# Kernel tuning notes

Measured on AMD Instinct MI355X. Metric: run time of the kernel, lower is better.

The kernel has to match this reference:

```python
import jax, jax.numpy as jnp
import numpy as np

NUM_HEADS = 16
ROPE_BASE = 10000.0


def _rope_interleaved(x, cos, sin):
    # x: [B,S,H,Hd]; cos/sin: [S,Hd/2]. Interleaved pairs (even, odd).
    x1 = x[..., 0::2]
    x2 = x[..., 1::2]
    c = cos[None, :, None, :]
    s = sin[None, :, None, :]
    o1 = x1 * c - x2 * s
    o2 = x1 * s + x2 * c
    return jnp.stack([o1, o2], axis=-1).reshape(x.shape)


def setup_inputs() -> dict:
    key = jax.random.key(0)
    ks = jax.random.split(key, 5)
    B, S, D = 2, 2048, 2048
    init_scale = 0.02
    x = jax.random.normal(ks[0], (B, S, D), jnp.float32)
    Wq = jax.random.normal(ks[1], (D, D), jnp.float32) * init_scale
    Wk = jax.random.normal(ks[2], (D, D), jnp.float32) * init_scale
    Wv = jax.random.normal(ks[3], (D, D), jnp.float32) * init_scale
    Wo = jax.random.normal(ks[4], (D, D), jnp.float32) * init_scale
    return {"x": x, "Wq": Wq, "Wk": Wk, "Wv": Wv, "Wo": Wo}


def reference(x, Wq, Wk, Wv, Wo):
    B, S, D = x.shape
    H = NUM_HEADS
    Hd = D // H
    # QKV projections (bias-free)
    q = (x @ Wq).reshape(B, S, H, Hd)
    k = (x @ Wk).reshape(B, S, H, Hd)
    v = (x @ Wv).reshape(B, S, H, Hd)
    # Rotary embedding, interleaved, base 10000, full head_dim
    pos = jnp.arange(S, dtype=jnp.float32)
    inv_freq = 1.0 / (ROPE_BASE ** (jnp.arange(0, Hd, 2, dtype=jnp.float32) / Hd))
    angles = pos[:, None] * inv_freq[None, :]  # [S, Hd/2]
    cos, sin = jnp.cos(angles), jnp.sin(angles)
    q = _rope_interleaved(q, cos, sin)
    k = _rope_interleaved(k, cos, sin)
    # Causal scaled-dot-product attention (flash_attn_func default scale = Hd**-0.5)
    scale = Hd ** -0.5
    scores = jnp.einsum('bqhd,bkhd->bhqk', q, k) * scale
    causal = jnp.tril(jnp.ones((S, S), dtype=bool))
    scores = jnp.where(causal[None, None], scores, jnp.finfo(scores.dtype).min)
    probs = jax.nn.softmax(scores, axis=-1)
    attn = jnp.einsum('bhqk,bkhd->bqhd', probs, v).reshape(B, S, D)
    return attn @ Wo
```

## Files before the change

kernel.cpp:

```cpp
#include <hip/hip_runtime.h>
#include <hip/hip_bf16.h>

static constexpr int BB = 2;
static constexpr int SS = 2048;
static constexpr int DD = 2048;
static constexpr int HH = 16;
static constexpr int HD = 128;

typedef __bf16 bf16_t;
typedef __bf16 bf16x8 __attribute__((ext_vector_type(8)));
typedef __bf16 bf16x4 __attribute__((ext_vector_type(4)));
typedef float  floatx4 __attribute__((ext_vector_type(4)));

__device__ __forceinline__ void gl2lds16(const bf16_t* g, bf16_t* l) {
    __builtin_amdgcn_global_load_lds(
        (const __attribute__((address_space(1))) void*)g,
        (__attribute__((address_space(3))) void*)l, 16, 0, 0);
}

__global__ void cast_x_kernel(const float* __restrict__ x, bf16_t* __restrict__ xb) {
    int i = blockIdx.x * 256 + threadIdx.x;
    float4 v = ((const float4*)x)[i];
    bf16x4 o;
    o.x = (bf16_t)v.x; o.y = (bf16_t)v.y; o.z = (bf16_t)v.z; o.w = (bf16_t)v.w;
    ((bf16x4*)xb)[i] = o;
}

__global__ void transpose_cast_kernel(const float* __restrict__ W, bf16_t* __restrict__ Wt) {
    __shared__ float tile[32][33];
    int bx = blockIdx.x * 32;
    int by = blockIdx.y * 32;
    int tx = threadIdx.x, ty = threadIdx.y;
#pragma unroll
    for (int j = 0; j < 4; ++j)
        tile[ty + j * 8][tx] = W[(size_t)(by + ty + j * 8) * DD + bx + tx];
    __syncthreads();
#pragma unroll
    for (int j = 0; j < 4; ++j)
        Wt[(size_t)(bx + ty + j * 8) * DD + by + tx] = (bf16_t)tile[tx][ty + j * 8];
}

template <int MODE>
__global__ __launch_bounds__(256, 2) void gemm_bt_kernel(
    const bf16_t* __restrict__ A, const bf16_t* __restrict__ Bt,
    float* __restrict__ Cf, bf16_t* __restrict__ Qw, bf16_t* __restrict__ Kw,
    bf16_t* __restrict__ Vtw, int N, int K) {
    __shared__ __align__(16) bf16_t As[128 * 64];
    __shared__ __align__(16) bf16_t Bs[128 * 64];

    const int t = threadIdx.x;
    const int lane = t & 63;
    const int wave = t >> 6;
    const int lrow = lane & 15;
    const int lkq  = lane >> 4;
    const int wm = (wave & 1) * 64;
    const int wn = (wave >> 1) * 64;
    const int m0 = blockIdx.y * 128;
    const int n0 = blockIdx.x * 128;

    floatx4 acc[4][4];
#pragma unroll
    for (int i = 0; i < 4; ++i)
#pragma unroll
        for (int j = 0; j < 4; ++j) acc[i][j] = (floatx4)0.0f;

    const int srow  = lane >> 3;
    const int sch   = (lane & 7) ^ srow;

    for (int k0 = 0; k0 < K; k0 += 64) {
        __syncthreads();
#pragma unroll
        for (int p = 0; p < 4; ++p) {
            int r = wave * 32 + p * 8 + srow;
            gl2lds16(A  + (size_t)(m0 + r) * K + k0 + sch * 8, As + (wave * 32 + p * 8) * 64);
            gl2lds16(Bt + (size_t)(n0 + r) * K + k0 + sch * 8, Bs + (wave * 32 + p * 8) * 64);
        }
        __syncthreads();
#pragma unroll
        for (int ks = 0; ks < 2; ++ks) {
            bf16x8 af[4], bg[4];
#pragma unroll
            for (int i = 0; i < 4; ++i) {
                int pos = ((ks * 4 + lkq) ^ (lrow & 7)) * 8;
                af[i] = *(const bf16x8*)(As + (wm + i * 16 + lrow) * 64 + pos);
                bg[i] = *(const bf16x8*)(Bs + (wn + i * 16 + lrow) * 64 + pos);
            }
#pragma unroll
            for (int i = 0; i < 4; ++i)
#pragma unroll
                for (int j = 0; j < 4; ++j)
                    acc[i][j] = __builtin_amdgcn_mfma_f32_16x16x32_bf16(af[i], bg[j], acc[i][j], 0, 0, 0);
        }
    }

#pragma unroll
    for (int i = 0; i < 4; ++i)
#pragma unroll
        for (int j = 0; j < 4; ++j)
#pragma unroll
            for (int r = 0; r < 4; ++r) {
                int m = m0 + wm + i * 16 + lkq * 4 + r;
                int n = n0 + wn + j * 16 + lrow;
                float v = acc[i][j][r];
                if (MODE == 1) {
                    Cf[(size_t)m * N + n] = v;
                } else {
                    bf16_t bv = (bf16_t)v;
                    int b = m >> 11, s = m & (SS - 1);
                    if (n < DD) {
                        int h = n >> 7, d = n & 127;
                        Qw[(((size_t)b * HH + h) * SS + s) * HD + d] = bv;
                    } else if (n < 2 * DD) {
                        int nn = n - DD;
                        int h = nn >> 7, d = nn & 127;
                        Kw[(((size_t)b * HH + h) * SS + s) * HD + d] = bv;
                    } else {
                        int nn = n - 2 * DD;
                        int h = nn >> 7, d = nn & 127;
                        Vtw[(((size_t)b * HH + h) * HD + d) * SS + s] = bv;
                    }
                }
            }
}

__global__ void rope_kernel(bf16_t* __restrict__ Qw, bf16_t* __restrict__ Kw) {
    int idx = blockIdx.x * 256 + threadIdx.x;
    int i  = idx & 63;
    int s  = (idx >> 6) & (SS - 1);
    int bh = idx >> 17;
    float inv = expf(-(float)(2 * i) * (9.210340371976184f / 128.0f));
    float ang = (float)s * inv;
    float c = cosf(ang), sn = sinf(ang);
    size_t base = ((size_t)bh * SS + s) * HD + 2 * i;
    float q1 = (float)Qw[base], q2 = (float)Qw[base + 1];
    Qw[base]     = (bf16_t)(q1 * c - q2 * sn);
    Qw[base + 1] = (bf16_t)(q1 * sn + q2 * c);
    float k1 = (float)Kw[base], k2 = (float)Kw[base + 1];
    Kw[base]     = (bf16_t)(k1 * c - k2 * sn);
    Kw[base + 1] = (bf16_t)(k1 * sn + k2 * c);
}

__global__ __launch_bounds__(256, 3) void flash_attn_kernel(
    const bf16_t* __restrict__ Qw, const bf16_t* __restrict__ Kw,
    const bf16_t* __restrict__ Vtw, bf16_t* __restrict__ Attn) {
    __shared__ __align__(16) bf16_t Ks[64 * 128];
    __shared__ __align__(16) bf16_t Vs[128 * 64];
    __shared__ __align__(16) bf16_t Ps[4][16 * 72];

    const int t = threadIdx.x;
    const int lane = t & 63;
    const int wave = t >> 6;
    const int lrow = lane & 15;
    const int lkq  = lane >> 4;
    const int bx = blockIdx.x;
    const int qtile = (bx & 1) ? (bx >> 1) : (15 - (bx >> 1));
    const int bh = blockIdx.y;
    const int q0 = qtile * 128;

    const bf16_t* Qbh = Qw + (size_t)bh * SS * HD;
    const bf16_t* Kbh = Kw + (size_t)bh * SS * HD;
    const bf16_t* Vbh = Vtw + (size_t)bh * HD * SS;

    const int qb[2] = { q0 + wave * 16, q0 + 64 + wave * 16 };

    const float qscale = 0.08838834764831845f * 1.4426950408889634f;
    bf16x8 qf[2][4];
#pragma unroll
    for (int qs = 0; qs < 2; ++qs)
#pragma unroll
        for (int kc4 = 0; kc4 < 4; ++kc4) {
            qf[qs][kc4] = *(const bf16x8*)(Qbh + (size_t)(qb[qs] + lrow) * HD + kc4 * 32 + lkq * 8);
#pragma unroll
            for (int e = 0; e < 8; ++e) qf[qs][kc4][e] = (bf16_t)((float)qf[qs][kc4][e] * qscale);
        }

    floatx4 oacc[2][8];
#pragma unroll
    for (int qs = 0; qs < 2; ++qs)
#pragma unroll
        for (int i = 0; i < 8; ++i) oacc[qs][i] = (floatx4)0.0f;
    float m_i[2] = { -1e30f, -1e30f };
    float l_i[2] = { 0.0f, 0.0f };

    const int nch = 2 * qtile + 2;
    for (int kc = 0; kc < nch; ++kc) {
        __syncthreads();
#pragma unroll
        for (int p = 0; p < 4; ++p) {
            int row = wave * 16 + p * 4 + (lane >> 4);
            int gch = (lane & 15) ^ (row & 7);
            gl2lds16(Kbh + (size_t)(kc * 64 + row) * HD + gch * 8,
                     Ks + (wave * 16 + p * 4) * 128);
        }
#pragma unroll
        for (int p = 0; p < 4; ++p) {
            int row = wave * 32 + p * 8 + (lane >> 3);
            int gch = (lane & 7) ^ (row & 7);
            gl2lds16(Vbh + (size_t)row * SS + kc * 64 + gch * 8,
                     Vs + (wave * 32 + p * 8) * 64);
        }
        __syncthreads();

#pragma unroll
        for (int qs = 0; qs < 2; ++qs) {
            const int qbase = qb[qs];
            if (kc * 64 > qbase + 15) continue;

            floatx4 sacc[4];
#pragma unroll
            for (int i = 0; i < 4; ++i) sacc[i] = (floatx4)0.0f;
#pragma unroll
            for (int nf = 0; nf < 4; ++nf)
#pragma unroll
                for (int kc4 = 0; kc4 < 4; ++kc4) {
                    bf16x8 kf = *(const bf16x8*)(Ks + (nf * 16 + lrow) * 128 +
                                                 (((kc4 * 4 + lkq) ^ (lrow & 7)) * 8));
                    sacc[nf] = __builtin_amdgcn_mfma_f32_16x16x32_bf16(kf, qf[qs][kc4], sacc[nf], 0, 0, 0);
                }

            const int qg = qbase + lrow;
            float mx = m_i[qs];
            if (kc * 64 + 63 > qbase) {
#pragma unroll
                for (int nf = 0; nf < 4; ++nf)
#pragma unroll
                    for (int r = 0; r < 4; ++r) {
                        int kg = kc * 64 + nf * 16 + lkq * 4 + r;
                        float sv = (kg > qg) ? -1e30f : sacc[nf][r];
                        sacc[nf][r] = sv;
                        mx = fmaxf(mx, sv);
                    }
            } else {
#pragma unroll
                for (int nf = 0; nf < 4; ++nf)
#pragma unroll
                    for (int r = 0; r < 4; ++r) mx = fmaxf(mx, sacc[nf][r]);
            }
            mx = fmaxf(mx, __shfl_xor(mx, 16));
            mx = fmaxf(mx, __shfl_xor(mx, 32));
            float alpha = exp2f(m_i[qs] - mx);
            m_i[qs] = mx;

            float rs = 0.0f;
#pragma unroll
            for (int nf = 0; nf < 4; ++nf)
#pragma unroll
                for (int r = 0; r < 4; ++r) {
                    float pv = exp2f(sacc[nf][r] - mx);
                    sacc[nf][r] = pv;
                    rs += pv;
                }
            rs += __shfl_xor(rs, 16);
            rs += __shfl_xor(rs, 32);
            l_i[qs] = l_i[qs] * alpha + rs;

            float av[4];
#pragma unroll
            for (int r = 0; r < 4; ++r) av[r] = __shfl(alpha, lkq * 4 + r);
#pragma unroll
            for (int nf8 = 0; nf8 < 8; ++nf8)
#pragma unroll
                for (int r = 0; r < 4; ++r) oacc[qs][nf8][r] *= av[r];

#pragma unroll
            for (int nf = 0; nf < 4; ++nf) {
                bf16x4 pk;
#pragma unroll
                for (int r = 0; r < 4; ++r) pk[r] = (bf16_t)sacc[nf][r];
                *(bf16x4*)(Ps[wave] + lrow * 72 + nf * 16 + lkq * 4) = pk;
            }

            bf16x8 pa[2];
#pragma unroll
            for (int k2 = 0; k2 < 2; ++k2)
                pa[k2] = *(const bf16x8*)(Ps[wave] + lrow * 72 + k2 * 32 + lkq * 8);
#pragma unroll
            for (int nf8 = 0; nf8 < 8; ++nf8)
#pragma unroll
                for (int k2 = 0; k2 < 2; ++k2) {
                    bf16x8 vb = *(const bf16x8*)(Vs + (nf8 * 16 + lrow) * 64 +
                                                 (((k2 * 4 + lkq) ^ (lrow & 7)) * 8));
                    oacc[qs][nf8] = __builtin_amdgcn_mfma_f32_16x16x32_bf16(pa[k2], vb, oacc[qs][nf8], 0, 0, 0);
                }
        }
    }

    int bb = bh >> 4, h = bh & 15;
#pragma unroll
    for (int qs = 0; qs < 2; ++qs)
#pragma unroll
        for (int r = 0; r < 4; ++r) {
            float invl = 1.0f / __shfl(l_i[qs], lkq * 4 + r);
            int q = qb[qs] + lkq * 4 + r;
#pragma unroll
            for (int nf8 = 0; nf8 < 8; ++nf8)
                Attn[((size_t)bb * SS + q) * DD + h * HD + nf8 * 16 + lrow] =
                    (bf16_t)(oacc[qs][nf8][r] * invl);
        }
}

extern "C" void kernel_launch(void* const* d_in, const int* in_sizes, int n_in,
                              void* d_out, int out_size, void* d_ws, size_t ws_size,
                              hipStream_t stream) {
    const float* x  = (const float*)d_in[0];
    const float* Wq = (const float*)d_in[1];
    const float* Wk = (const float*)d_in[2];
    const float* Wv = (const float*)d_in[3];
    const float* Wo = (const float*)d_in[4];
    float* out = (float*)d_out;

    bf16_t* p = (bf16_t*)d_ws;
    bf16_t* Xb    = p; p += (size_t)BB * SS * DD;
    bf16_t* Wqkvt = p; p += (size_t)3 * DD * DD;
    bf16_t* Wot   = p; p += (size_t)DD * DD;
    bf16_t* Qw    = p; p += (size_t)BB * HH * SS * HD;
    bf16_t* Kw    = p; p += (size_t)BB * HH * SS * HD;
    bf16_t* Vtw   = p; p += (size_t)BB * HH * SS * HD;
    bf16_t* Attn  = p; p += (size_t)BB * SS * DD;

    cast_x_kernel<<<(BB * SS * DD / 4) / 256, 256, 0, stream>>>(x, Xb);

    dim3 tb(32, 8), tg(DD / 32, DD / 32);
    transpose_cast_kernel<<<tg, tb, 0, stream>>>(Wq, Wqkvt);
    transpose_cast_kernel<<<tg, tb, 0, stream>>>(Wk, Wqkvt + (size_t)DD * DD);
    transpose_cast_kernel<<<tg, tb, 0, stream>>>(Wv, Wqkvt + (size_t)2 * DD * DD);
    transpose_cast_kernel<<<tg, tb, 0, stream>>>(Wo, Wot);

    gemm_bt_kernel<0><<<dim3(3 * DD / 128, BB * SS / 128), 256, 0, stream>>>(
        Xb, Wqkvt, nullptr, Qw, Kw, Vtw, 3 * DD, DD);

    rope_kernel<<<(BB * HH * SS * 64) / 256, 256, 0, stream>>>(Qw, Kw);

    flash_attn_kernel<<<dim3(SS / 128, BB * HH), 256, 0, stream>>>(Qw, Kw, Vtw, Attn);

    gemm_bt_kernel<1><<<dim3(DD / 128, BB * SS / 128), 256, 0, stream>>>(
        Attn, Wot, out, nullptr, nullptr, nullptr, DD, DD);
}
```

Before: 445.5 us.

## Load K/V fragments directly into registers, dropping shared-memory staging in flash attention

The flash attention loop no longer stages K and V tiles through LDS with block-wide barriers. Each wave now loads its K and V MFMA fragments straight from global memory into registers and reuses them for both query sub-tiles. The rescale of the output accumulator is skipped when no lane's running max changed. This removes two __syncthreads per chunk and the LDS round trip, but every wave now fetches the full K/V tile from global memory or L2 (four times the global traffic), and register pressure grows, so launch bounds drop from 3 to 2 blocks.

```diff
diff --git a/kernel.cpp b/kernel.cpp
--- a/kernel.cpp
+++ b/kernel.cpp
@@ -140,11 +140,9 @@
     Kw[base + 1] = (bf16_t)(k1 * sn + k2 * c);
 }
 
-__global__ __launch_bounds__(256, 3) void flash_attn_kernel(
+__global__ __launch_bounds__(256, 2) void flash_attn_kernel(
     const bf16_t* __restrict__ Qw, const bf16_t* __restrict__ Kw,
     const bf16_t* __restrict__ Vtw, bf16_t* __restrict__ Attn) {
-    __shared__ __align__(16) bf16_t Ks[64 * 128];
-    __shared__ __align__(16) bf16_t Vs[128 * 64];
     __shared__ __align__(16) bf16_t Ps[4][16 * 72];
 
     const int t = threadIdx.x;
@@ -184,39 +182,42 @@
 
     const int nch = 2 * qtile + 2;
     for (int kc = 0; kc < nch; ++kc) {
-        __syncthreads();
-#pragma unroll
-        for (int p = 0; p < 4; ++p) {
-            int row = wave * 16 + p * 4 + (lane >> 4);
-            int gch = (lane & 15) ^ (row & 7);
-            gl2lds16(Kbh + (size_t)(kc * 64 + row) * HD + gch * 8,
-                     Ks + (wave * 16 + p * 4) * 128);
-        }
-#pragma unroll
-        for (int p = 0; p < 4; ++p) {
-            int row = wave * 32 + p * 8 + (lane >> 3);
-            int gch = (lane & 7) ^ (row & 7);
-            gl2lds16(Vbh + (size_t)row * SS + kc * 64 + gch * 8,
-                     Vs + (wave * 32 + p * 8) * 64);
-        }
-        __syncthreads();
+        bf16x8 kf[4][4];
+#pragma unroll
+        for (int nf = 0; nf < 4; ++nf)
+#pragma unroll
+            for (int kc4 = 0; kc4 < 4; ++kc4)
+                kf[nf][kc4] = *(const bf16x8*)(Kbh + (size_t)(kc * 64 + nf * 16 + lrow) * HD +
+                                               kc4 * 32 + lkq * 8);
+
+        const bool act0 = (kc * 64 <= qb[0] + 15);
+
+        floatx4 sacc[2][4];
+#pragma unroll
+        for (int qs = 0; qs < 2; ++qs)
+#pragma unroll
+            for (int i = 0; i < 4; ++i) sacc[qs][i] = (floatx4)0.0f;
+#pragma unroll
+        for (int nf = 0; nf < 4; ++nf)
+#pragma unroll
+            for (int kc4 = 0; kc4 < 4; ++kc4) {
+                if (act0)
+                    sacc[0][nf] = __builtin_amdgcn_mfma_f32_16x16x32_bf16(kf[nf][kc4], qf[0][kc4], sacc[0][nf], 0, 0, 0);
+                sacc[1][nf] = __builtin_amdgcn_mfma_f32_16x16x32_bf16(kf[nf][kc4], qf[1][kc4], sacc[1][nf], 0, 0, 0);
+            }
+
+        bf16x8 vf[8][2];
+#pragma unroll
+        for (int nf8 = 0; nf8 < 8; ++nf8)
+#pragma unroll
+            for (int k2 = 0; k2 < 2; ++k2)
+                vf[nf8][k2] = *(const bf16x8*)(Vbh + (size_t)(nf8 * 16 + lrow) * SS +
+                                               kc * 64 + k2 * 32 + lkq * 8);
 
 #pragma unroll
         for (int qs = 0; qs < 2; ++qs) {
             const int qbase = qb[qs];
-            if (kc * 64 > qbase + 15) continue;
-
-            floatx4 sacc[4];
-#pragma unroll
-            for (int i = 0; i < 4; ++i) sacc[i] = (floatx4)0.0f;
-#pragma unroll
-            for (int nf = 0; nf < 4; ++nf)
-#pragma unroll
-                for (int kc4 = 0; kc4 < 4; ++kc4) {
-                    bf16x8 kf = *(const bf16x8*)(Ks + (nf * 16 + lrow) * 128 +
-                                                 (((kc4 * 4 + lkq) ^ (lrow & 7)) * 8));
-                    sacc[nf] = __builtin_amdgcn_mfma_f32_16x16x32_bf16(kf, qf[qs][kc4], sacc[nf], 0, 0, 0);
-                }
+            if (qs == 0 && !act0) continue;
 
             const int qg = qbase + lrow;
             float mx = m_i[qs];
@@ -226,15 +227,15 @@
 #pragma unroll
                     for (int r = 0; r < 4; ++r) {
                         int kg = kc * 64 + nf * 16 + lkq * 4 + r;
-                        float sv = (kg > qg) ? -1e30f : sacc[nf][r];
-                        sacc[nf][r] = sv;
+                        float sv = (kg > qg) ? -1e30f : sacc[qs][nf][r];
+                        sacc[qs][nf][r] = sv;
                         mx = fmaxf(mx, sv);
                     }
             } else {
 #pragma unroll
                 for (int nf = 0; nf < 4; ++nf)
 #pragma unroll
-                    for (int r = 0; r < 4; ++r) mx = fmaxf(mx, sacc[nf][r]);
+                    for (int r = 0; r < 4; ++r) mx = fmaxf(mx, sacc[qs][nf][r]);
             }
             mx = fmaxf(mx, __shfl_xor(mx, 16));
             mx = fmaxf(mx, __shfl_xor(mx, 32));
@@ -246,27 +247,29 @@
             for (int nf = 0; nf < 4; ++nf)
 #pragma unroll
                 for (int r = 0; r < 4; ++r) {
-                    float pv = exp2f(sacc[nf][r] - mx);
-                    sacc[nf][r] = pv;
+                    float pv = exp2f(sacc[qs][nf][r] - mx);
+                    sacc[qs][nf][r] = pv;
                     rs += pv;
                 }
             rs += __shfl_xor(rs, 16);
             rs += __shfl_xor(rs, 32);
             l_i[qs] = l_i[qs] * alpha + rs;
 
-            float av[4];
-#pragma unroll
-            for (int r = 0; r < 4; ++r) av[r] = __shfl(alpha, lkq * 4 + r);
-#pragma unroll
-            for (int nf8 = 0; nf8 < 8; ++nf8)
-#pragma unroll
-                for (int r = 0; r < 4; ++r) oacc[qs][nf8][r] *= av[r];
+            if (__ballot(alpha < 1.0f)) {
+                float av[4];
+#pragma unroll
+                for (int r = 0; r < 4; ++r) av[r] = __shfl(alpha, lkq * 4 + r);
+#pragma unroll
+                for (int nf8 = 0; nf8 < 8; ++nf8)
+#pragma unroll
+                    for (int r = 0; r < 4; ++r) oacc[qs][nf8][r] *= av[r];
+            }
 
 #pragma unroll
             for (int nf = 0; nf < 4; ++nf) {
                 bf16x4 pk;
 #pragma unroll
-                for (int r = 0; r < 4; ++r) pk[r] = (bf16_t)sacc[nf][r];
+                for (int r = 0; r < 4; ++r) pk[r] = (bf16_t)sacc[qs][nf][r];
                 *(bf16x4*)(Ps[wave] + lrow * 72 + nf * 16 + lkq * 4) = pk;
             }
 
@@ -277,11 +280,8 @@
 #pragma unroll
             for (int nf8 = 0; nf8 < 8; ++nf8)
 #pragma unroll
-                for (int k2 = 0; k2 < 2; ++k2) {
-                    bf16x8 vb = *(const bf16x8*)(Vs + (nf8 * 16 + lrow) * 64 +
-                                                 (((k2 * 4 + lkq) ^ (lrow & 7)) * 8));
-                    oacc[qs][nf8] = __builtin_amdgcn_mfma_f32_16x16x32_bf16(pa[k2], vb, oacc[qs][nf8], 0, 0, 0);
-                }
+                for (int k2 = 0; k2 < 2; ++k2)
+                    oacc[qs][nf8] = __builtin_amdgcn_mfma_f32_16x16x32_bf16(pa[k2], vf[nf8][k2], oacc[qs][nf8], 0, 0, 0);
         }
     }
 
```

Result: slower. 562.2 us (+26.2%).

## Interleave two q-subtiles in flash attention, skip no-op rescale, separate V transpose

Applied to the files above, without the earlier changes.

The QKV GEMM now writes V in row-major head layout, so its epilogue no longer does strided scattered stores, and a separate tiled LDS kernel transposes V into the layout attention expects. The attention inner loop now computes both q-subtiles' QK and PV MFMAs together, sharing each K/V fragment load across two accumulators. It also skips the output rescale when no lane's running max changed. This adds a kernel launch and an extra pass over V, and lowers launch bounds occupancy from 3 to 2 blocks per CU to make room for more live registers.

```diff
diff --git a/kernel.cpp b/kernel.cpp
--- a/kernel.cpp
+++ b/kernel.cpp
@@ -44,7 +44,7 @@
 __global__ __launch_bounds__(256, 2) void gemm_bt_kernel(
     const bf16_t* __restrict__ A, const bf16_t* __restrict__ Bt,
     float* __restrict__ Cf, bf16_t* __restrict__ Qw, bf16_t* __restrict__ Kw,
-    bf16_t* __restrict__ Vtw, int N, int K) {
+    bf16_t* __restrict__ Vw, int N, int K) {
     __shared__ __align__(16) bf16_t As[128 * 64];
     __shared__ __align__(16) bf16_t Bs[128 * 64];
 
@@ -107,18 +107,12 @@
                 } else {
                     bf16_t bv = (bf16_t)v;
                     int b = m >> 11, s = m & (SS - 1);
-                    if (n < DD) {
-                        int h = n >> 7, d = n & 127;
-                        Qw[(((size_t)b * HH + h) * SS + s) * HD + d] = bv;
-                    } else if (n < 2 * DD) {
-                        int nn = n - DD;
-                        int h = nn >> 7, d = nn & 127;
-                        Kw[(((size_t)b * HH + h) * SS + s) * HD + d] = bv;
-                    } else {
-                        int nn = n - 2 * DD;
-                        int h = nn >> 7, d = nn & 127;
-                        Vtw[(((size_t)b * HH + h) * HD + d) * SS + s] = bv;
-                    }
+                    int nn = n & (DD - 1);
+                    int h = nn >> 7, d = nn & 127;
+                    size_t off = (((size_t)b * HH + h) * SS + s) * HD + d;
+                    if (n < DD)            Qw[off] = bv;
+                    else if (n < 2 * DD)   Kw[off] = bv;
+                    else                   Vw[off] = bv;
                 }
             }
 }
@@ -140,7 +134,34 @@
     Kw[base + 1] = (bf16_t)(k1 * sn + k2 * c);
 }
 
-__global__ __launch_bounds__(256, 3) void flash_attn_kernel(
+__global__ void vtrans_kernel(const bf16_t* __restrict__ Vw, bf16_t* __restrict__ Vt) {
+    __shared__ unsigned short lds[64][65];
+    const int t = threadIdx.x;
+    const int s0 = blockIdx.x * 64, d0 = blockIdx.y * 64, bh = blockIdx.z;
+    const bf16_t* src = Vw + ((size_t)bh * SS + s0) * HD + d0;
+    bf16_t* dst = Vt + ((size_t)bh * HD + d0) * SS + s0;
+#pragma unroll
+    for (int p = 0; p < 2; ++p) {
+        int c = p * 256 + t;
+        int s = c >> 3, ch = c & 7;
+        uint4 v = *(const uint4*)(src + (size_t)s * HD + ch * 8);
+        const unsigned short* pv = (const unsigned short*)&v;
+#pragma unroll
+        for (int e = 0; e < 8; ++e) lds[ch * 8 + e][s] = pv[e];
+    }
+    __syncthreads();
+    {
+        int d = t >> 2, sb = (t & 3) * 16;
+        uint4 o[2];
+        unsigned short* po = (unsigned short*)o;
+#pragma unroll
+        for (int e = 0; e < 16; ++e) po[e] = lds[d][sb + e];
+        *(uint4*)(dst + (size_t)d * SS + sb) = o[0];
+        *(uint4*)(dst + (size_t)d * SS + sb + 8) = o[1];
+    }
+}
+
+__global__ __launch_bounds__(256, 2) void flash_attn_kernel(
     const bf16_t* __restrict__ Qw, const bf16_t* __restrict__ Kw,
     const bf16_t* __restrict__ Vtw, bf16_t* __restrict__ Attn) {
     __shared__ __align__(16) bf16_t Ks[64 * 128];
@@ -201,22 +222,29 @@
         }
         __syncthreads();
 
+        const bool act0 = (kc * 64 <= qb[0] + 15);
+
+        floatx4 sacc[2][4];
+#pragma unroll
+        for (int qs = 0; qs < 2; ++qs)
+#pragma unroll
+            for (int i = 0; i < 4; ++i) sacc[qs][i] = (floatx4)0.0f;
+#pragma unroll
+        for (int nf = 0; nf < 4; ++nf)
+#pragma unroll
+            for (int kc4 = 0; kc4 < 4; ++kc4) {
+                bf16x8 kf = *(const bf16x8*)(Ks + (nf * 16 + lrow) * 128 +
+                                             (((kc4 * 4 + lkq) ^ (lrow & 7)) * 8));
+                if (act0)
+                    sacc[0][nf] = __builtin_amdgcn_mfma_f32_16x16x32_bf16(kf, qf[0][kc4], sacc[0][nf], 0, 0, 0);
+                sacc[1][nf] = __builtin_amdgcn_mfma_f32_16x16x32_bf16(kf, qf[1][kc4], sacc[1][nf], 0, 0, 0);
+            }
+
+        bf16x8 pa[2][2];
 #pragma unroll
         for (int qs = 0; qs < 2; ++qs) {
             const int qbase = qb[qs];
-            if (kc * 64 > qbase + 15) continue;
-
-            floatx4 sacc[4];
-#pragma unroll
-            for (int i = 0; i < 4; ++i) sacc[i] = (floatx4)0.0f;
-#pragma unroll
-            for (int nf = 0; nf < 4; ++nf)
-#pragma unroll
-                for (int kc4 = 0; kc4 < 4; ++kc4) {
-                    bf16x8 kf = *(const bf16x8*)(Ks + (nf * 16 + lrow) * 128 +
-                                                 (((kc4 * 4 + lkq) ^ (lrow & 7)) * 8));
-                    sacc[nf] = __builtin_amdgcn_mfma_f32_16x16x32_bf16(kf, qf[qs][kc4], sacc[nf], 0, 0, 0);
-                }
+            if (qs == 0 && !act0) continue;
 
             const int qg = qbase + lrow;
             float mx = m_i[qs];
@@ -226,15 +254,15 @@
 #pragma unroll
                     for (int r = 0; r < 4; ++r) {
                         int kg = kc * 64 + nf * 16 + lkq * 4 + r;
-                        float sv = (kg > qg) ? -1e30f : sacc[nf][r];
-                        sacc[nf][r] = sv;
+                        float sv = (kg > qg) ? -1e30f : sacc[qs][nf][r];
+                        sacc[qs][nf][r] = sv;
                         mx = fmaxf(mx, sv);
                     }
             } else {
 #pragma unroll
                 for (int nf = 0; nf < 4; ++nf)
 #pragma unroll
-                    for (int r = 0; r < 4; ++r) mx = fmaxf(mx, sacc[nf][r]);
+                    for (int r = 0; r < 4; ++r) mx = fmaxf(mx, sacc[qs][nf][r]);
             }
             mx = fmaxf(mx, __shfl_xor(mx, 16));
             mx = fmaxf(mx, __shfl_xor(mx, 32));
@@ -246,43 +274,46 @@
             for (int nf = 0; nf < 4; ++nf)
 #pragma unroll
                 for (int r = 0; r < 4; ++r) {
-                    float pv = exp2f(sacc[nf][r] - mx);
-                    sacc[nf][r] = pv;
+                    float pv = exp2f(sacc[qs][nf][r] - mx);
+                    sacc[qs][nf][r] = pv;
                     rs += pv;
                 }
             rs += __shfl_xor(rs, 16);
             rs += __shfl_xor(rs, 32);
             l_i[qs] = l_i[qs] * alpha + rs;
 
-            float av[4];
-#pragma unroll
-            for (int r = 0; r < 4; ++r) av[r] = __shfl(alpha, lkq * 4 + r);
-#pragma unroll
-            for (int nf8 = 0; nf8 < 8; ++nf8)
-#pragma unroll
-                for (int r = 0; r < 4; ++r) oacc[qs][nf8][r] *= av[r];
+            if (__ballot(alpha < 1.0f)) {
+                float av[4];
+#pragma unroll
+                for (int r = 0; r < 4; ++r) av[r] = __shfl(alpha, lkq * 4 + r);
+#pragma unroll
+                for (int nf8 = 0; nf8 < 8; ++nf8)
+#pragma unroll
+                    for (int r = 0; r < 4; ++r) oacc[qs][nf8][r] *= av[r];
+            }
 
 #pragma unroll
             for (int nf = 0; nf < 4; ++nf) {
                 bf16x4 pk;
 #pragma unroll
-                for (int r = 0; r < 4; ++r) pk[r] = (bf16_t)sacc[nf][r];
+                for (int r = 0; r < 4; ++r) pk[r] = (bf16_t)sacc[qs][nf][r];
                 *(bf16x4*)(Ps[wave] + lrow * 72 + nf * 16 + lkq * 4) = pk;
             }
-
-            bf16x8 pa[2];
 #pragma unroll
             for (int k2 = 0; k2 < 2; ++k2)
-                pa[k2] = *(const bf16x8*)(Ps[wave] + lrow * 72 + k2 * 32 + lkq * 8);
-#pragma unroll
-            for (int nf8 = 0; nf8 < 8; ++nf8)
-#pragma unroll
-                for (int k2 = 0; k2 < 2; ++k2) {
-                    bf16x8 vb = *(const bf16x8*)(Vs + (nf8 * 16 + lrow) * 64 +
-                                                 (((k2 * 4 + lkq) ^ (lrow & 7)) * 8));
-                    oacc[qs][nf8] = __builtin_amdgcn_mfma_f32_16x16x32_bf16(pa[k2], vb, oacc[qs][nf8], 0, 0, 0);
-                }
-        }
+                pa[qs][k2] = *(const bf16x8*)(Ps[wave] + lrow * 72 + k2 * 32 + lkq * 8);
+        }
+
+#pragma unroll
+        for (int nf8 = 0; nf8 < 8; ++nf8)
+#pragma unroll
+            for (int k2 = 0; k2 < 2; ++k2) {
+                bf16x8 vf = *(const bf16x8*)(Vs + (nf8 * 16 + lrow) * 64 +
+                                             (((k2 * 4 + lkq) ^ (lrow & 7)) * 8));
+                if (act0)
+                    oacc[0][nf8] = __builtin_amdgcn_mfma_f32_16x16x32_bf16(pa[0][k2], vf, oacc[0][nf8], 0, 0, 0);
+                oacc[1][nf8] = __builtin_amdgcn_mfma_f32_16x16x32_bf16(pa[1][k2], vf, oacc[1][nf8], 0, 0, 0);
+            }
     }
 
     int bb = bh >> 4, h = bh & 15;
@@ -317,6 +348,7 @@
     bf16_t* Kw    = p; p += (size_t)BB * HH * SS * HD;
     bf16_t* Vtw   = p; p += (size_t)BB * HH * SS * HD;
     bf16_t* Attn  = p; p += (size_t)BB * SS * DD;
+    bf16_t* Vw = Attn;
 
     cast_x_kernel<<<(BB * SS * DD / 4) / 256, 256, 0, stream>>>(x, Xb);
 
@@ -327,9 +359,11 @@
     transpose_cast_kernel<<<tg, tb, 0, stream>>>(Wo, Wot);
 
     gemm_bt_kernel<0><<<dim3(3 * DD / 128, BB * SS / 128), 256, 0, stream>>>(
-        Xb, Wqkvt, nullptr, Qw, Kw, Vtw, 3 * DD, DD);
+        Xb, Wqkvt, nullptr, Qw, Kw, Vw, 3 * DD, DD);
 
     rope_kernel<<<(BB * HH * SS * 64) / 256, 256, 0, stream>>>(Qw, Kw);
+
+    vtrans_kernel<<<dim3(SS / 64, HD / 64, BB * HH), 256, 0, stream>>>(Vw, Vtw);
 
     flash_attn_kernel<<<dim3(SS / 128, BB * HH), 256, 0, stream>>>(Qw, Kw, Vtw, Attn);
 
```

Result: faster. 411.0 us (-7.7%).
